# Optimization experiments

Measured on AMD Instinct MI355X. Metric: run time of the kernel, lower is better.

Reference implementation:

```python
import jax, jax.numpy as jnp
import numpy as np

BATCH, LENGTH, IN, STATE, OUT = 8, 4096, 512, 256, 512


def setup_inputs() -> dict:
    key = jax.random.key(0)
    k1, k2, k3, k4, k5 = jax.random.split(key, 5)
    u = jax.random.normal(k1, (BATCH, LENGTH, IN), dtype=jnp.float32)
    x0 = jax.random.normal(k2, (BATCH, STATE), dtype=jnp.float32)
    A = 0.9999 * (2.0 * jax.random.uniform(k3, (STATE,), dtype=jnp.float32) - 1.0)
    B = jax.random.normal(k4, (IN, STATE), dtype=jnp.float32) / (STATE + IN) ** 0.5
    C = jax.random.normal(k5, (STATE, OUT), dtype=jnp.float32) / STATE ** 0.5
    return {"u": u, "x0": x0, "A": A, "B": B, "C": C}


def reference(u, x0, A, B, C):
    L = u.shape[1]
    # A_powers[t, n] = A[n] ** t, shape [L, state]
    A_powers = jnp.power(A[None, :], jnp.arange(L, dtype=u.dtype)[:, None])
    uB = u @ B  # [batch, L, state]
    # FFT convolution; inputs are real so rfft/irfft gives same result as
    # real(ifft(fft*fft)) in the original.
    T = 2 ** int(np.ceil(np.log2(2 * L - 1)))
    Af = jnp.fft.rfft(A_powers, n=T, axis=0)  # [T/2+1, state]
    Uf = jnp.fft.rfft(uB, n=T, axis=1)        # [batch, T/2+1, state]
    x = jnp.fft.irfft(Af[None, :, :] * Uf, n=T, axis=1)[:, :L]  # [batch, L, state]
    # initial-state contribution: A * A_powers * x0
    x = x + A[None, None, :] * A_powers[None, :, :] * x0[:, None, :]
    y = x @ C  # [batch, L, out]
    return (y, x[:, -1])
```

## Files before the change

kernel.cpp:

```cpp
#include <hip/hip_runtime.h>

#define BATCH   8
#define LENGTH  4096
#define IN_DIM  512
#define STATE   256
#define OUT_DIM 512
#define NC      64
#define LC      64

typedef __attribute__((ext_vector_type(8))) short bf16x8;
typedef __attribute__((ext_vector_type(4))) float f32x4;

union FragU { bf16x8 v; unsigned u[4]; };

__device__ __forceinline__ unsigned short bf16_rne(float v) {
    unsigned u = __builtin_bit_cast(unsigned, v);
    unsigned r = (u + 0x7FFFu + ((u >> 16) & 1u)) >> 16;
    return (unsigned short)r;
}
__device__ __forceinline__ float bf16_f(unsigned short h) {
    unsigned u = ((unsigned)h) << 16;
    return __builtin_bit_cast(float, u);
}

__global__ __launch_bounds__(256) void split_weights(
    const float* __restrict__ B, const float* __restrict__ C,
    unsigned short* __restrict__ Bhi, unsigned short* __restrict__ Blo,
    unsigned short* __restrict__ Chi, unsigned short* __restrict__ Clo)
{
    int id = blockIdx.x * 256 + threadIdx.x;
    if (id < IN_DIM * STATE) {
        int k = id & (IN_DIM - 1), n = id >> 9;
        float v = B[(size_t)k * STATE + n];
        unsigned short h = bf16_rne(v);
        Bhi[id] = h;
        Blo[id] = bf16_rne(v - bf16_f(h));
    } else {
        int id2 = id - IN_DIM * STATE;
        int k = id2 & (STATE - 1), n = id2 >> 8;
        float v = C[(size_t)k * OUT_DIM + n];
        unsigned short h = bf16_rne(v);
        Chi[id2] = h;
        Clo[id2] = bf16_rne(v - bf16_f(h));
    }
}

__global__ __launch_bounds__(512, 4) void gemm_dbuf(
    const float* __restrict__ Af, const unsigned short* __restrict__ Bthi,
    const unsigned short* __restrict__ Btlo, float* __restrict__ Cc,
    int N_, int K)
{
    __shared__ unsigned short lds[2 * 16384];

    const int tid  = threadIdx.x;
    const int wave = tid >> 6;
    const int lane = tid & 63;
    const int n0 = blockIdx.x * 128;
    const int m0 = blockIdx.y * 128;

    const char* gp[4];
    int ldsoff[4], gstep[4];
    #pragma unroll
    for (int t = 0; t < 4; ++t) {
        int gi = wave * 4 + t;
        if (gi < 16) {
            int p = gi * 64 + lane;
            int row = p >> 3, s = p & 7;
            int l = s ^ (row & 7);
            gp[t] = (const char*)(Af + (size_t)(m0 + row) * K + l * 4);
            gstep[t] = 32 * 4;
            ldsoff[t] = gi * 512;
        } else {
            int q2 = (gi - 16) >> 3;
            int pi = gi & 7;
            int p = pi * 64 + lane;
            int row = p >> 2, s = p & 3;
            int l = s ^ ((row >> 1) & 3);
            const unsigned short* base = q2 ? Btlo : Bthi;
            gp[t] = (const char*)(base + (size_t)(n0 + row) * K + l * 8);
            gstep[t] = 32 * 2;
            ldsoff[t] = 8192 + q2 * 4096 + pi * 512;
        }
    }

    const int r = lane & 15, q = lane >> 4;
    const int wm = (wave >> 1) * 32, wn = (wave & 1) * 64;

    int aoff[2][2], boff[4];
    #pragma unroll
    for (int i = 0; i < 2; ++i) {
        int row = wm + i * 16 + r;
        #pragma unroll
        for (int h = 0; h < 2; ++h)
            aoff[i][h] = row * 64 + ((2 * q + h) ^ (row & 7)) * 8;
    }
    #pragma unroll
    for (int j = 0; j < 4; ++j) {
        int row = wn + j * 16 + r;
        boff[j] = row * 32 + (q ^ ((row >> 1) & 3)) * 8;
    }

    f32x4 acc[2][4];
    #pragma unroll
    for (int i = 0; i < 2; ++i)
        #pragma unroll
        for (int j = 0; j < 4; ++j)
            acc[i][j] = (f32x4){0.f, 0.f, 0.f, 0.f};

    #pragma unroll
    for (int t = 0; t < 4; ++t) {
        __builtin_amdgcn_global_load_lds(
            (const __attribute__((address_space(1))) unsigned*)(gp[t]),
            (__attribute__((address_space(3))) unsigned*)(&lds[ldsoff[t]]),
            16, 0, 0);
        gp[t] += gstep[t];
    }

    const int nit = K >> 5;
    for (int it = 0; it < nit; ++it) {
        asm volatile("" ::: "memory");
        __builtin_amdgcn_s_barrier();
        asm volatile("" ::: "memory");
        if (it + 1 < nit) {
            const int bb = ((it + 1) & 1) * 16384;
            #pragma unroll
            for (int t = 0; t < 4; ++t) {
                __builtin_amdgcn_global_load_lds(
                    (const __attribute__((address_space(1))) unsigned*)(gp[t]),
                    (__attribute__((address_space(3))) unsigned*)(&lds[bb + ldsoff[t]]),
                    16, 0, 0);
                gp[t] += gstep[t];
            }
            __builtin_amdgcn_s_waitcnt(0x0F74);
        } else {
            __builtin_amdgcn_s_waitcnt(0x0F70);
        }
        asm volatile("" ::: "memory");
        __builtin_amdgcn_s_barrier();
        asm volatile("" ::: "memory");

        const unsigned short* buf = &lds[(it & 1) * 16384];

        FragU ahi[2], alo[2];
        #pragma unroll
        for (int i = 0; i < 2; ++i) {
            #pragma unroll
            for (int h = 0; h < 2; ++h) {
                float4 f = *(const float4*)(buf + aoff[i][h]);
                unsigned bx = __builtin_bit_cast(unsigned, f.x);
                unsigned by = __builtin_bit_cast(unsigned, f.y);
                unsigned bz = __builtin_bit_cast(unsigned, f.z);
                unsigned bw = __builtin_bit_cast(unsigned, f.w);
                ahi[i].u[h * 2]     = __builtin_amdgcn_perm(by, bx, 0x07060302);
                ahi[i].u[h * 2 + 1] = __builtin_amdgcn_perm(bw, bz, 0x07060302);
                float lx = f.x - __builtin_bit_cast(float, bx & 0xFFFF0000u);
                float ly = f.y - __builtin_bit_cast(float, by & 0xFFFF0000u);
                float lz = f.z - __builtin_bit_cast(float, bz & 0xFFFF0000u);
                float lw = f.w - __builtin_bit_cast(float, bw & 0xFFFF0000u);
                alo[i].u[h * 2]     = __builtin_amdgcn_perm(
                    __builtin_bit_cast(unsigned, ly), __builtin_bit_cast(unsigned, lx), 0x07060302);
                alo[i].u[h * 2 + 1] = __builtin_amdgcn_perm(
                    __builtin_bit_cast(unsigned, lw), __builtin_bit_cast(unsigned, lz), 0x07060302);
            }
        }
        FragU bhi[4], blo[4];
        #pragma unroll
        for (int j = 0; j < 4; ++j) {
            bhi[j].v = *(const bf16x8*)(buf +  8192 + boff[j]);
            blo[j].v = *(const bf16x8*)(buf + 12288 + boff[j]);
        }
        #pragma unroll
        for (int i = 0; i < 2; ++i)
            #pragma unroll
            for (int j = 0; j < 4; ++j) {
                acc[i][j] = __builtin_amdgcn_mfma_f32_16x16x32_bf16(ahi[i].v, bhi[j].v, acc[i][j], 0, 0, 0);
                acc[i][j] = __builtin_amdgcn_mfma_f32_16x16x32_bf16(alo[i].v, bhi[j].v, acc[i][j], 0, 0, 0);
                acc[i][j] = __builtin_amdgcn_mfma_f32_16x16x32_bf16(ahi[i].v, blo[j].v, acc[i][j], 0, 0, 0);
            }
    }

    #pragma unroll
    for (int i = 0; i < 2; ++i) {
        #pragma unroll
        for (int reg = 0; reg < 4; ++reg) {
            int mg = m0 + wm + i * 16 + q * 4 + reg;
            float* dst = Cc + (size_t)mg * N_ + n0 + wn + r;
            dst[0]  = acc[i][0][reg];
            dst[16] = acc[i][1][reg];
            dst[32] = acc[i][2][reg];
            dst[48] = acc[i][3][reg];
        }
    }
}

__global__ __launch_bounds__(512, 4) void gemm_presplit(
    const unsigned short* __restrict__ Athi, const unsigned short* __restrict__ Atlo,
    const unsigned short* __restrict__ Bthi, const unsigned short* __restrict__ Btlo,
    float* __restrict__ Cc, int N_, int K)
{
    __shared__ unsigned short lds[2 * 16384];

    const int tid  = threadIdx.x;
    const int wave = tid >> 6;
    const int lane = tid & 63;
    const int n0 = blockIdx.x * 128;
    const int m0 = blockIdx.y * 128;

    const char* gp[4];
    int ldsoff[4];
    #pragma unroll
    for (int t = 0; t < 4; ++t) {
        int gi = wave * 4 + t;
        int plane = gi >> 3;
        int pi = gi & 7;
        int p = pi * 64 + lane;
        int row = p >> 2, s = p & 3;
        int l = s ^ ((row >> 1) & 3);
        const unsigned short* base =
            (plane == 0) ? Athi : (plane == 1) ? Atlo : (plane == 2) ? Bthi : Btlo;
        int r0 = (plane < 2) ? m0 : n0;
        gp[t] = (const char*)(base + (size_t)(r0 + row) * K + l * 8);
        ldsoff[t] = plane * 4096 + pi * 512;
    }

    const int r = lane & 15, q = lane >> 4;
    const int wm = (wave >> 2) * 64, wn = (wave & 3) * 32;

    int aoff[4], boff[2];
    #pragma unroll
    for (int i = 0; i < 4; ++i) {
        int row = wm + i * 16 + r;
        aoff[i] = row * 32 + (q ^ ((row >> 1) & 3)) * 8;
    }
    #pragma unroll
    for (int j = 0; j < 2; ++j) {
        int row = wn + j * 16 + r;
        boff[j] = row * 32 + (q ^ ((row >> 1) & 3)) * 8;
    }

    f32x4 acc[4][2];
    #pragma unroll
    for (int i = 0; i < 4; ++i)
        #pragma unroll
        for (int j = 0; j < 2; ++j)
            acc[i][j] = (f32x4){0.f, 0.f, 0.f, 0.f};

    #pragma unroll
    for (int t = 0; t < 4; ++t) {
        __builtin_amdgcn_global_load_lds(
            (const __attribute__((address_space(1))) unsigned*)(gp[t]),
            (__attribute__((address_space(3))) unsigned*)(&lds[ldsoff[t]]),
            16, 0, 0);
        gp[t] += 64;
    }

    const int nit = K >> 5;
    for (int it = 0; it < nit; ++it) {
        asm volatile("" ::: "memory");
        __builtin_amdgcn_s_barrier();
        asm volatile("" ::: "memory");
        if (it + 1 < nit) {
            const int bb = ((it + 1) & 1) * 16384;
            #pragma unroll
            for (int t = 0; t < 4; ++t) {
                __builtin_amdgcn_global_load_lds(
                    (const __attribute__((address_space(1))) unsigned*)(gp[t]),
                    (__attribute__((address_space(3))) unsigned*)(&lds[bb + ldsoff[t]]),
                    16, 0, 0);
                gp[t] += 64;
            }
            __builtin_amdgcn_s_waitcnt(0x0F74);
        } else {
            __builtin_amdgcn_s_waitcnt(0x0F70);
        }
        asm volatile("" ::: "memory");
        __builtin_amdgcn_s_barrier();
        asm volatile("" ::: "memory");

        const unsigned short* buf = &lds[(it & 1) * 16384];

        FragU ahi[4], alo[4];
        #pragma unroll
        for (int i = 0; i < 4; ++i) {
            ahi[i].v = *(const bf16x8*)(buf +        aoff[i]);
            alo[i].v = *(const bf16x8*)(buf + 4096 + aoff[i]);
        }
        FragU bhi[2], blo[2];
        #pragma unroll
        for (int j = 0; j < 2; ++j) {
            bhi[j].v = *(const bf16x8*)(buf +  8192 + boff[j]);
            blo[j].v = *(const bf16x8*)(buf + 12288 + boff[j]);
        }
        #pragma unroll
        for (int i = 0; i < 4; ++i)
            #pragma unroll
            for (int j = 0; j < 2; ++j) {
                acc[i][j] = __builtin_amdgcn_mfma_f32_16x16x32_bf16(ahi[i].v, bhi[j].v, acc[i][j], 0, 0, 0);
                acc[i][j] = __builtin_amdgcn_mfma_f32_16x16x32_bf16(alo[i].v, bhi[j].v, acc[i][j], 0, 0, 0);
                acc[i][j] = __builtin_amdgcn_mfma_f32_16x16x32_bf16(ahi[i].v, blo[j].v, acc[i][j], 0, 0, 0);
            }
    }

    #pragma unroll
    for (int i = 0; i < 4; ++i) {
        #pragma unroll
        for (int reg = 0; reg < 4; ++reg) {
            int mg = m0 + wm + i * 16 + q * 4 + reg;
            float* dst = Cc + (size_t)mg * N_ + n0 + wn + r;
            dst[0]  = acc[i][0][reg];
            dst[16] = acc[i][1][reg];
        }
    }
}

__global__ __launch_bounds__(256) void scan_carry(
    const float* __restrict__ uB, const float* __restrict__ A,
    float* __restrict__ carry)
{
    const int b = blockIdx.x;
    const int c = blockIdx.y;
    const int n = threadIdx.x;
    const float a = A[n];
    const float* p = uB + ((size_t)b * LENGTH + (size_t)c * LC) * STATE + n;
    float s = 0.f;
    #pragma unroll 8
    for (int j = 0; j < LC; ++j) s = a * s + p[(size_t)j * STATE];
    carry[((size_t)b * NC + c) * STATE + n] = s;
}

__global__ __launch_bounds__(256) void scan_apply(
    const float* __restrict__ uB, const float* __restrict__ A,
    const float* __restrict__ carry, const float* __restrict__ x0,
    unsigned short* __restrict__ xhi, unsigned short* __restrict__ xlo,
    float* __restrict__ x_last)
{
    const int b = blockIdx.x;
    const int c = blockIdx.y;
    const int n = threadIdx.x;
    const float a = A[n];
    float a2 = a * a, a4 = a2 * a2, a8 = a4 * a4, a16 = a8 * a8, a32 = a16 * a16;
    const float aLC = a32 * a32;

    float s = x0[(size_t)b * STATE + n];
    for (int d = 0; d < c; ++d)
        s = aLC * s + carry[((size_t)b * NC + d) * STATE + n];

    const size_t base = ((size_t)b * LENGTH + (size_t)c * LC) * STATE + n;
    const float* p = uB + base;
    unsigned short* qh = xhi + base;
    unsigned short* ql = xlo + base;
    #pragma unroll 8
    for (int j = 0; j < LC; ++j) {
        s = a * s + p[(size_t)j * STATE];
        unsigned u = __builtin_bit_cast(unsigned, s);
        qh[(size_t)j * STATE] = (unsigned short)(u >> 16);
        float lo = s - __builtin_bit_cast(float, u & 0xFFFF0000u);
        ql[(size_t)j * STATE] = (unsigned short)(__builtin_bit_cast(unsigned, lo) >> 16);
    }
    if (c == NC - 1) x_last[(size_t)b * STATE + n] = s;
}

extern "C" void kernel_launch(void* const* d_in, const int* in_sizes, int n_in,
                              void* d_out, int out_size, void* d_ws, size_t ws_size,
                              hipStream_t stream)
{
    const float* u  = (const float*)d_in[0];
    const float* x0 = (const float*)d_in[1];
    const float* A  = (const float*)d_in[2];
    const float* B  = (const float*)d_in[3];
    const float* C  = (const float*)d_in[4];

    const size_t MB = 1024 * 1024;
    char* ws = (char*)d_ws;

    unsigned short* xhi = (unsigned short*)(ws);
    unsigned short* xlo = (unsigned short*)(ws + 16 * MB);
    float* carry = (float*)(ws + 32 * MB);
    unsigned short* Bt_hi = (unsigned short*)(ws + 33 * MB);
    unsigned short* Bt_lo = (unsigned short*)(ws + 33 * MB + 256 * 1024);
    unsigned short* Ct_hi = (unsigned short*)(ws + 33 * MB + 512 * 1024);
    unsigned short* Ct_lo = (unsigned short*)(ws + 33 * MB + 768 * 1024);

    float* y      = (float*)d_out;
    float* x_last = y + (size_t)BATCH * LENGTH * OUT_DIM;
    float* uB     = (float*)((char*)d_out + 32 * MB);

    const int M = BATCH * LENGTH;

    split_weights<<<dim3((IN_DIM * STATE + STATE * OUT_DIM) / 256), dim3(256), 0, stream>>>(
        B, C, Bt_hi, Bt_lo, Ct_hi, Ct_lo);

    gemm_dbuf<<<dim3(STATE / 128, M / 128), dim3(512), 0, stream>>>(
        u, Bt_hi, Bt_lo, uB, STATE, IN_DIM);

    scan_carry<<<dim3(BATCH, NC), dim3(256), 0, stream>>>(uB, A, carry);
    scan_apply<<<dim3(BATCH, NC), dim3(256), 0, stream>>>(uB, A, carry, x0, xhi, xlo, x_last);

    gemm_presplit<<<dim3(OUT_DIM / 128, M / 128), dim3(512), 0, stream>>>(
        xhi, xlo, Ct_hi, Ct_lo, y, OUT_DIM, STATE);
}
```

Measured before the change: 200.0 us.

## Shorten scan chunks, vectorize scan kernels with float4, swizzle GEMM workgroups per XCD

The scan switches from 64 chunks of length 64 to 256 chunks of length 16. Each thread now handles four state channels with float4 loads and packed 4x16-bit stores, which shortens the serial dependency chains and widens memory accesses. Both GEMMs remap workgroup indices so consecutive tiles land on the same XCD for better L2 reuse. In exchange, scan_apply's sequential carry-prefix loop can now run up to 255 iterations for late chunks, and the carry buffer grows, so the weight buffers are moved to new workspace offsets.

```diff
diff --git a/kernel.cpp b/kernel.cpp
--- a/kernel.cpp
+++ b/kernel.cpp
@@ -5,11 +5,12 @@
 #define IN_DIM  512
 #define STATE   256
 #define OUT_DIM 512
-#define NC      64
-#define LC      64
+#define NC      256
+#define LC      16
 
 typedef __attribute__((ext_vector_type(8))) short bf16x8;
 typedef __attribute__((ext_vector_type(4))) float f32x4;
+typedef __attribute__((ext_vector_type(4))) unsigned short u16x4;
 
 union FragU { bf16x8 v; unsigned u[4]; };
 
@@ -55,8 +56,13 @@
     const int tid  = threadIdx.x;
     const int wave = tid >> 6;
     const int lane = tid & 63;
-    const int n0 = blockIdx.x * 128;
-    const int m0 = blockIdx.y * 128;
+
+    const unsigned nwgx = gridDim.x;
+    const unsigned flat = blockIdx.y * nwgx + blockIdx.x;
+    const unsigned cpx  = (nwgx * gridDim.y) >> 3;
+    const unsigned swz  = (flat & 7u) * cpx + (flat >> 3);
+    const int n0 = (int)(swz % nwgx) * 128;
+    const int m0 = (int)(swz / nwgx) * 128;
 
     const char* gp[4];
     int ldsoff[4], gstep[4];
@@ -203,8 +209,13 @@
     const int tid  = threadIdx.x;
     const int wave = tid >> 6;
     const int lane = tid & 63;
-    const int n0 = blockIdx.x * 128;
-    const int m0 = blockIdx.y * 128;
+
+    const unsigned nwgx = gridDim.x;
+    const unsigned flat = blockIdx.y * nwgx + blockIdx.x;
+    const unsigned cpx  = (nwgx * gridDim.y) >> 3;
+    const unsigned swz  = (flat & 7u) * cpx + (flat >> 3);
+    const int n0 = (int)(swz % nwgx) * 128;
+    const int m0 = (int)(swz / nwgx) * 128;
 
     const char* gp[4];
     int ldsoff[4];
@@ -313,22 +324,28 @@
     }
 }
 
-__global__ __launch_bounds__(256) void scan_carry(
+__global__ __launch_bounds__(64) void scan_carry(
     const float* __restrict__ uB, const float* __restrict__ A,
     float* __restrict__ carry)
 {
     const int b = blockIdx.x;
     const int c = blockIdx.y;
-    const int n = threadIdx.x;
-    const float a = A[n];
-    const float* p = uB + ((size_t)b * LENGTH + (size_t)c * LC) * STATE + n;
-    float s = 0.f;
-    #pragma unroll 8
-    for (int j = 0; j < LC; ++j) s = a * s + p[(size_t)j * STATE];
-    carry[((size_t)b * NC + c) * STATE + n] = s;
-}
-
-__global__ __launch_bounds__(256) void scan_apply(
+    const int t = threadIdx.x;
+    const float4 a = *(const float4*)(A + 4 * t);
+    const float4* p = (const float4*)(uB + ((size_t)b * LENGTH + (size_t)c * LC) * STATE) + t;
+    float4 s = make_float4(0.f, 0.f, 0.f, 0.f);
+    #pragma unroll
+    for (int j = 0; j < LC; ++j) {
+        float4 v = p[(size_t)j * (STATE / 4)];
+        s.x = fmaf(a.x, s.x, v.x);
+        s.y = fmaf(a.y, s.y, v.y);
+        s.z = fmaf(a.z, s.z, v.z);
+        s.w = fmaf(a.w, s.w, v.w);
+    }
+    *((float4*)(carry + ((size_t)b * NC + c) * STATE) + t) = s;
+}
+
+__global__ __launch_bounds__(64) void scan_apply(
     const float* __restrict__ uB, const float* __restrict__ A,
     const float* __restrict__ carry, const float* __restrict__ x0,
     unsigned short* __restrict__ xhi, unsigned short* __restrict__ xlo,
@@ -336,28 +353,57 @@
 {
     const int b = blockIdx.x;
     const int c = blockIdx.y;
-    const int n = threadIdx.x;
-    const float a = A[n];
-    float a2 = a * a, a4 = a2 * a2, a8 = a4 * a4, a16 = a8 * a8, a32 = a16 * a16;
-    const float aLC = a32 * a32;
-
-    float s = x0[(size_t)b * STATE + n];
-    for (int d = 0; d < c; ++d)
-        s = aLC * s + carry[((size_t)b * NC + d) * STATE + n];
-
-    const size_t base = ((size_t)b * LENGTH + (size_t)c * LC) * STATE + n;
-    const float* p = uB + base;
-    unsigned short* qh = xhi + base;
-    unsigned short* ql = xlo + base;
-    #pragma unroll 8
+    const int t = threadIdx.x;
+    const float4 a = *(const float4*)(A + 4 * t);
+    float4 aL = a;
+    #pragma unroll
+    for (int k = 0; k < 4; ++k) {
+        aL.x *= aL.x; aL.y *= aL.y; aL.z *= aL.z; aL.w *= aL.w;
+    }
+
+    float4 s = *((const float4*)(x0 + (size_t)b * STATE) + t);
+    const float4* cr = (const float4*)(carry + (size_t)b * NC * STATE) + t;
+    for (int d = 0; d < c; ++d) {
+        float4 v = cr[(size_t)d * (STATE / 4)];
+        s.x = fmaf(aL.x, s.x, v.x);
+        s.y = fmaf(aL.y, s.y, v.y);
+        s.z = fmaf(aL.z, s.z, v.z);
+        s.w = fmaf(aL.w, s.w, v.w);
+    }
+
+    const size_t base = ((size_t)b * LENGTH + (size_t)c * LC) * STATE;
+    const float4* p = (const float4*)(uB + base) + t;
+    u16x4* qh = (u16x4*)(xhi + base) + t;
+    u16x4* ql = (u16x4*)(xlo + base) + t;
+    #pragma unroll
     for (int j = 0; j < LC; ++j) {
-        s = a * s + p[(size_t)j * STATE];
-        unsigned u = __builtin_bit_cast(unsigned, s);
-        qh[(size_t)j * STATE] = (unsigned short)(u >> 16);
-        float lo = s - __builtin_bit_cast(float, u & 0xFFFF0000u);
-        ql[(size_t)j * STATE] = (unsigned short)(__builtin_bit_cast(unsigned, lo) >> 16);
-    }
-    if (c == NC - 1) x_last[(size_t)b * STATE + n] = s;
+        float4 v = p[(size_t)j * (STATE / 4)];
+        s.x = fmaf(a.x, s.x, v.x);
+        s.y = fmaf(a.y, s.y, v.y);
+        s.z = fmaf(a.z, s.z, v.z);
+        s.w = fmaf(a.w, s.w, v.w);
+        u16x4 hh, ll;
+        unsigned ux = __builtin_bit_cast(unsigned, s.x);
+        unsigned uy = __builtin_bit_cast(unsigned, s.y);
+        unsigned uz = __builtin_bit_cast(unsigned, s.z);
+        unsigned uw = __builtin_bit_cast(unsigned, s.w);
+        hh[0] = (unsigned short)(ux >> 16);
+        hh[1] = (unsigned short)(uy >> 16);
+        hh[2] = (unsigned short)(uz >> 16);
+        hh[3] = (unsigned short)(uw >> 16);
+        float lx = s.x - __builtin_bit_cast(float, ux & 0xFFFF0000u);
+        float ly = s.y - __builtin_bit_cast(float, uy & 0xFFFF0000u);
+        float lz = s.z - __builtin_bit_cast(float, uz & 0xFFFF0000u);
+        float lw = s.w - __builtin_bit_cast(float, uw & 0xFFFF0000u);
+        ll[0] = (unsigned short)(__builtin_bit_cast(unsigned, lx) >> 16);
+        ll[1] = (unsigned short)(__builtin_bit_cast(unsigned, ly) >> 16);
+        ll[2] = (unsigned short)(__builtin_bit_cast(unsigned, lz) >> 16);
+        ll[3] = (unsigned short)(__builtin_bit_cast(unsigned, lw) >> 16);
+        qh[(size_t)j * (STATE / 4)] = hh;
+        ql[(size_t)j * (STATE / 4)] = ll;
+    }
+    if (c == NC - 1)
+        *((float4*)(x_last + (size_t)b * STATE) + t) = s;
 }
 
 extern "C" void kernel_launch(void* const* d_in, const int* in_sizes, int n_in,
@@ -376,10 +422,10 @@
     unsigned short* xhi = (unsigned short*)(ws);
     unsigned short* xlo = (unsigned short*)(ws + 16 * MB);
     float* carry = (float*)(ws + 32 * MB);
-    unsigned short* Bt_hi = (unsigned short*)(ws + 33 * MB);
-    unsigned short* Bt_lo = (unsigned short*)(ws + 33 * MB + 256 * 1024);
-    unsigned short* Ct_hi = (unsigned short*)(ws + 33 * MB + 512 * 1024);
-    unsigned short* Ct_lo = (unsigned short*)(ws + 33 * MB + 768 * 1024);
+    unsigned short* Bt_hi = (unsigned short*)(ws + 34 * MB);
+    unsigned short* Bt_lo = (unsigned short*)(ws + 34 * MB + 256 * 1024);
+    unsigned short* Ct_hi = (unsigned short*)(ws + 34 * MB + 512 * 1024);
+    unsigned short* Ct_lo = (unsigned short*)(ws + 34 * MB + 768 * 1024);
 
     float* y      = (float*)d_out;
     float* x_last = y + (size_t)BATCH * LENGTH * OUT_DIM;
@@ -393,8 +439,8 @@
     gemm_dbuf<<<dim3(STATE / 128, M / 128), dim3(512), 0, stream>>>(
         u, Bt_hi, Bt_lo, uB, STATE, IN_DIM);
 
-    scan_carry<<<dim3(BATCH, NC), dim3(256), 0, stream>>>(uB, A, carry);
-    scan_apply<<<dim3(BATCH, NC), dim3(256), 0, stream>>>(uB, A, carry, x0, xhi, xlo, x_last);
+    scan_carry<<<dim3(BATCH, NC), dim3(64), 0, stream>>>(uB, A, carry);
+    scan_apply<<<dim3(BATCH, NC), dim3(64), 0, stream>>>(uB, A, carry, x0, xhi, xlo, x_last);
 
     gemm_presplit<<<dim3(OUT_DIM / 128, M / 128), dim3(512), 0, stream>>>(
         xhi, xlo, Ct_hi, Ct_lo, y, OUT_DIM, STATE);
```

Measured after the change: 238.8 us. 19.4% more time.
